# Kernel tuning notes

Hardware: AMD Instinct MI355X
Metric: run time of the kernel (lower is better)

Reference implementation:

```python
import jax, jax.numpy as jnp
import numpy as np

D = 128
H = 4
DK = D // H


def _spmm(row, col, val, x, n):
    # sparse.mm(adj, x) with adj in COO form: out[row] += val * x[col]
    return jax.ops.segment_sum(val[:, None] * x[col], row, num_segments=n)


def _arrg(h, a1_w, a1_b, a2_w, a2_b):
    return jax.nn.leaky_relu(h @ a1_w + a1_b, negative_slope=0.01) @ a2_w + a2_b


def _cross_attn(x, q_x, q_w, k_w, v_w):
    n, d = x.shape
    m = q_x.shape[0]
    q = (q_x @ q_w).reshape(m, H, DK).transpose(1, 0, 2)   # [H, Q, dk]
    k = (x @ k_w).reshape(n, H, DK).transpose(1, 0, 2)     # [H, N, dk]
    v = (q_x @ v_w).reshape(m, H, DK).transpose(1, 0, 2)   # [H, Q, dk]
    s = jnp.einsum('hnd,hqd->hnq', k, q) / jnp.sqrt(jnp.float32(DK))
    w = jax.nn.softmax(s, axis=-1)                          # softmax over queries
    out = jnp.einsum('hnq,hqd->hnd', w, v).transpose(1, 0, 2).reshape(n, d)
    return out + x


def setup_inputs() -> dict:
    key = jax.random.key(0)
    ks = iter(jax.random.split(key, 64))
    nrm = lambda shape, s=0.05: jax.random.normal(next(ks), shape, jnp.float32) * s
    inp = {}
    inp['trans_w'] = nrm((1, D)); inp['trans_b'] = nrm((D,))
    inp['g_w'] = nrm((D, D));     inp['g_b'] = nrm((D,))
    inp['qg_w'] = nrm((D, D));    inp['qg_b'] = nrm((D,))
    inp['q_w'] = nrm((D, D)); inp['k_w'] = nrm((D, D)); inp['v_w'] = nrm((D, D))
    inp['a1_w'] = nrm((D, 2 * D)); inp['a1_b'] = nrm((2 * D,))
    inp['a2_w'] = nrm((2 * D, D)); inp['a2_b'] = nrm((D,))
    inp['x0'] = jax.random.normal(next(ks), (25000,), jnp.float32)
    inp['q0'] = jax.random.normal(next(ks), (100,), jnp.float32)
    for i in (1, 2, 3):
        inp[f'xin{i}'] = jax.random.normal(next(ks), (25000,), jnp.float32)
        inp[f'qin{i}'] = jax.random.normal(next(ks), (100,), jnp.float32)
    n_sizes = {1: 50000, 2: 75000, 3: 100000}
    q_sizes = {1: 200, 2: 300, 3: 400}
    for i in (1, 2, 3):
        e = 16 * n_sizes[i]
        inp[f'aval{i}'] = jax.random.uniform(next(ks), (e,), jnp.float32)
        inp[f'arow{i}'] = jax.random.randint(next(ks), (e,), 0, n_sizes[i], jnp.int64)
        inp[f'acol{i}'] = jax.random.randint(next(ks), (e,), 0, n_sizes[i], jnp.int64)
        qe = 16 * q_sizes[i]
        inp[f'qval{i}'] = jax.random.uniform(next(ks), (qe,), jnp.float32)
        inp[f'qrow{i}'] = jax.random.randint(next(ks), (qe,), 0, q_sizes[i], jnp.int64)
        inp[f'qcol{i}'] = jax.random.randint(next(ks), (qe,), 0, q_sizes[i], jnp.int64)
    return inp


def reference(trans_w, trans_b, g_w, g_b, qg_w, qg_b, q_w, k_w, v_w,
              a1_w, a1_b, a2_w, a2_b,
              x0, q0, xin1, xin2, xin3, qin1, qin2, qin3,
              aval1, aval2, aval3, qval1, qval2, qval3,
              arow1, acol1, arow2, acol2, arow3, acol3,
              qrow1, qcol1, qrow2, qcol2, qrow3, qcol3):
    trans = lambda v: v[:, None] @ trans_w + trans_b
    x = trans(x0)
    qx = trans(q0)
    steps = [
        (xin1, qin1, arow1, acol1, aval1, qrow1, qcol1, qval1, 50000, 200),
        (xin2, qin2, arow2, acol2, aval2, qrow2, qcol2, qval2, 75000, 300),
        (xin3, qin3, arow3, acol3, aval3, qrow3, qcol3, qval3, 100000, 400),
    ]
    for xin, qin, ar, ac, av, qr, qc, qv, n, m in steps:
        x = jnp.concatenate([x, trans(xin)], axis=0)
        qx = jnp.concatenate([qx, trans(qin)], axis=0)
        x = _spmm(ar, ac, av, x @ g_w + g_b, n)
        qx = _spmm(qr, qc, qv, qx @ qg_w + qg_b, m)
        x = _arrg(x, a1_w, a1_b, a2_w, a2_b)
        qx = _arrg(qx, a1_w, a1_b, a2_w, a2_b)
        x = _cross_attn(x, qx, q_w, k_w, v_w)
    return (x, qx)
```

## Files before the change

### kernel.cpp

```cpp
#include <hip/hip_runtime.h>

typedef unsigned short u16;
typedef __attribute__((ext_vector_type(8))) short bf16x8;
typedef __attribute__((ext_vector_type(4))) float f32x4;
typedef __attribute__((ext_vector_type(2))) unsigned u32x2;

__device__ __forceinline__ float b2f(u16 v) {
    return __uint_as_float(((unsigned)v) << 16);
}
__device__ __forceinline__ u16 f2b(float x) {
    unsigned u = __float_as_uint(x);
    unsigned r = u + 0x7FFFu + ((u >> 16) & 1u);
    return (u16)(r >> 16);
}
__device__ __forceinline__ float4 load_bf4(const u16* p) {
    ushort4 q = *(const ushort4*)p;
    float4 f;
    f.x = b2f(q.x); f.y = b2f(q.y); f.z = b2f(q.z); f.w = b2f(q.w);
    return f;
}
__device__ __forceinline__ float4 in4(const void* p, long off, bool bf) {
    if (bf) return load_bf4((const u16*)p + off);
    return *(const float4*)((const float*)p + off);
}
__device__ __forceinline__ float in1(const void* p, long off, bool bf) {
    if (bf) return b2f(((const u16*)p)[off]);
    return ((const float*)p)[off];
}
__device__ __forceinline__ int inIdx(const void* p, long i, bool i64) {
    return ((const int*)p)[i64 ? 2 * i : i];
}

__global__ void sniff_kernel(const u16* __restrict__ x0bits, const int* __restrict__ arow,
                             int* __restrict__ flags) {
    if (threadIdx.x != 0 || blockIdx.x != 0) return;
    int plaus = 0;
    for (int i = 0; i < 256; ++i) {
        u16 v = x0bits[i];
        int e = (v >> 7) & 0xFF;
        if (v == 0 || (e >= 100 && e <= 135)) plaus++;
    }
    flags[0] = (plaus >= 200) ? 1 : 0;
    int nz = 0;
    for (int i = 1; i < 128; i += 2) nz += (arow[i] != 0);
    flags[1] = (nz == 0) ? 1 : 0;
}

__global__ void trans2_kernel(const void* __restrict__ vx, float* __restrict__ outx, int rowsx,
                              const void* __restrict__ vq, float* __restrict__ outq, int rowsq,
                              const void* __restrict__ tw, const void* __restrict__ tb,
                              const int* __restrict__ flags) {
    const bool bf = flags[0] != 0;
    int t = blockIdx.x * blockDim.x + threadIdx.x;
    int c4 = (t & 31) * 4;
    int r = t >> 5;
    const void* v; float* out;
    if (r < rowsx) { v = vx; out = outx; }
    else { r -= rowsx; if (r >= rowsq) return; v = vq; out = outq; }
    float vv = in1(v, r, bf);
    float4 w4 = in4(tw, c4, bf);
    float4 b4 = in4(tb, c4, bf);
    float4 o;
    o.x = vv * w4.x + b4.x; o.y = vv * w4.y + b4.y;
    o.z = vv * w4.z + b4.z; o.w = vv * w4.w + b4.w;
    *(float4*)(out + (size_t)r * 128 + c4) = o;
}

__global__ void wprep_kernel(const void* __restrict__ src, u16* __restrict__ dst,
                             int K, int N, const int* __restrict__ flags) {
    const bool bf = flags[0] != 0;
    int idx = blockIdx.x * blockDim.x + threadIdx.x;
    if (idx >= K * N) return;
    int j = idx & 7, lane = (idx >> 3) & 63, t = idx >> 9;
    int KC = K >> 5;
    int kc = t % KC, ct = t / KC;
    int k = kc * 32 + (lane >> 4) * 8 + j;
    int nn = ct * 16 + (lane & 15);
    dst[idx] = f2b(in1(src, (long)k * N + nn, bf));
}

template<int KTOT, int NOUT, bool LEAKY, typename AT, typename CT>
__launch_bounds__(256)
__global__ void gemm_mfma_kernel(const AT* __restrict__ A, const u16* __restrict__ Wf,
                                 const void* __restrict__ bias, CT* __restrict__ C,
                                 int n, const int* __restrict__ flags) {
    constexpr int KC = KTOT / 32;
    constexpr int NT = NOUT / 16;
    __shared__ u16 wlds[KTOT * NOUT];
    {
        const int4* srcw = (const int4*)Wf;
        int4* dstw = (int4*)wlds;
        constexpr int NV = KTOT * NOUT * 2 / 16;
#pragma unroll
        for (int i = 0; i < NV / 256; ++i)
            dstw[i * 256 + threadIdx.x] = srcw[i * 256 + threadIdx.x];
    }
    __syncthreads();
    const bool bf = flags[0] != 0;
    const int lane = threadIdx.x & 63;
    const int wave = threadIdx.x >> 6;
    const int quad = lane >> 4, col = lane & 15;
    const int rbase = (blockIdx.x * 4 + wave) * 16;
    if (rbase >= n) return;
    int node = rbase + col; if (node >= n) node = n - 1;
    f32x4 acc[NT];
#pragma unroll
    for (int ct = 0; ct < NT; ++ct) acc[ct] = (f32x4){0.f, 0.f, 0.f, 0.f};
#pragma unroll
    for (int kc = 0; kc < KC; ++kc) {
        bf16x8 af;
        if constexpr (sizeof(AT) == 2) {
            af = *(const bf16x8*)((const u16*)A + (size_t)node * KTOT + kc * 32 + quad * 8);
        } else {
            const float* ap = (const float*)A + (size_t)node * KTOT + kc * 32 + quad * 8;
            float4 a0 = *(const float4*)ap;
            float4 a1 = *(const float4*)(ap + 4);
            af[0] = (short)f2b(a0.x); af[1] = (short)f2b(a0.y);
            af[2] = (short)f2b(a0.z); af[3] = (short)f2b(a0.w);
            af[4] = (short)f2b(a1.x); af[5] = (short)f2b(a1.y);
            af[6] = (short)f2b(a1.z); af[7] = (short)f2b(a1.w);
        }
#pragma unroll
        for (int ct = 0; ct < NT; ++ct) {
            bf16x8 wf = *(const bf16x8*)(wlds + (((ct * KC + kc) * 64 + lane) * 8));
            acc[ct] = __builtin_amdgcn_mfma_f32_16x16x32_bf16(af, wf, acc[ct], 0, 0, 0);
        }
    }
#pragma unroll
    for (int ct = 0; ct < NT; ++ct) {
        int colg = ct * 16 + col;
        float b = bias ? in1(bias, colg, bf) : 0.f;
#pragma unroll
        for (int r = 0; r < 4; ++r) {
            int row = rbase + quad * 4 + r;
            if (row >= n) continue;
            float v = acc[ct][r] + b;
            if (LEAKY) v = v > 0.f ? v : 0.01f * v;
            if constexpr (sizeof(CT) == 2) C[(size_t)row * NOUT + colg] = (CT)f2b(v);
            else                           C[(size_t)row * NOUT + colg] = (CT)v;
        }
    }
}

__launch_bounds__(256)
__global__ void gemm_qv_kernel(const float* __restrict__ A, const u16* __restrict__ Wfq,
                               const u16* __restrict__ Wfv, u16* __restrict__ Qf,
                               u16* __restrict__ Vf, int m, int mt32) {
    __shared__ u16 wldsq[128 * 128];
    __shared__ u16 wldsv[128 * 128];
    {
        const int4* sq = (const int4*)Wfq;
        const int4* sv = (const int4*)Wfv;
        int4* dq = (int4*)wldsq;
        int4* dv = (int4*)wldsv;
#pragma unroll
        for (int i = 0; i < 8; ++i) {
            dq[i * 256 + threadIdx.x] = sq[i * 256 + threadIdx.x];
            dv[i * 256 + threadIdx.x] = sv[i * 256 + threadIdx.x];
        }
    }
    __syncthreads();
    const int mpad = mt32 * 32;
    const int mt16 = mt32 * 2;
    const int lane = threadIdx.x & 63;
    const int wave = threadIdx.x >> 6;
    const int quad = lane >> 4, col = lane & 15;
    const int rbase = (blockIdx.x * 4 + wave) * 16;
    if (rbase >= mpad) return;
    int node = rbase + col; if (node >= m) node = m - 1;
    f32x4 accq[8], accv[8];
#pragma unroll
    for (int ct = 0; ct < 8; ++ct) {
        accq[ct] = (f32x4){0.f, 0.f, 0.f, 0.f};
        accv[ct] = (f32x4){0.f, 0.f, 0.f, 0.f};
    }
#pragma unroll
    for (int kc = 0; kc < 4; ++kc) {
        const float* ap = A + (size_t)node * 128 + kc * 32 + quad * 8;
        float4 a0 = *(const float4*)ap;
        float4 a1 = *(const float4*)(ap + 4);
        bf16x8 af;
        af[0] = (short)f2b(a0.x); af[1] = (short)f2b(a0.y);
        af[2] = (short)f2b(a0.z); af[3] = (short)f2b(a0.w);
        af[4] = (short)f2b(a1.x); af[5] = (short)f2b(a1.y);
        af[6] = (short)f2b(a1.z); af[7] = (short)f2b(a1.w);
#pragma unroll
        for (int ct = 0; ct < 8; ++ct) {
            bf16x8 wq = *(const bf16x8*)(wldsq + (((ct * 4 + kc) * 64 + lane) * 8));
            bf16x8 wv = *(const bf16x8*)(wldsv + (((ct * 4 + kc) * 64 + lane) * 8));
            accq[ct] = __builtin_amdgcn_mfma_f32_16x16x32_bf16(af, wq, accq[ct], 0, 0, 0);
            accv[ct] = __builtin_amdgcn_mfma_f32_16x16x32_bf16(af, wv, accv[ct], 0, 0, 0);
        }
    }
    const float qscale = 0.17677669529663687f * 1.44269504088896340736f;
#pragma unroll
    for (int ct = 0; ct < 8; ++ct) {
        int colg = ct * 16 + col;
        int h = colg >> 5, dim = colg & 31;
#pragma unroll
        for (int r = 0; r < 4; ++r) {
            int row = rbase + quad * 4 + r;
            if (row >= mpad) continue;
            bool pad = row >= m;
            float vq = pad ? 0.f : accq[ct][r] * qscale;
            float vv = pad ? 0.f : accv[ct][r];
            {
                size_t idx = ((((size_t)h * mt16 + (row >> 4)) * 64)
                              + ((dim >> 3) << 4) + (row & 15)) * 8 + (dim & 7);
                Qf[idx] = f2b(vq);
            }
            {
                size_t idx = (((((size_t)h * mt32 + (row >> 5)) * 2 + (dim >> 4)) * 64)
                              + (((row >> 3) & 3) << 4) + (dim & 15)) * 8 + (row & 7);
                Vf[idx] = f2b(vv);
            }
        }
    }
}

#define RSH 8
#define NBC_MAX 512
#define EPB 4096

__global__ void zero_int_kernel(int* __restrict__ p, int n) {
    int i = blockIdx.x * blockDim.x + threadIdx.x;
    if (i < n) p[i] = 0;
}

__global__ void bhist_kernel(const void* __restrict__ rows, int e, int* __restrict__ bcnt,
                             int nbc, const int* __restrict__ flags) {
    __shared__ int hist[NBC_MAX];
    const bool i64 = flags[1] != 0;
    for (int i = threadIdx.x; i < nbc; i += 256) hist[i] = 0;
    __syncthreads();
    int base = blockIdx.x * 8192;
    int end = base + 8192; if (end > e) end = e;
    for (int i = base + threadIdx.x; i < end; i += 256)
        atomicAdd(&hist[inIdx(rows, i, i64) >> RSH], 1);
    __syncthreads();
    for (int i = threadIdx.x; i < nbc; i += 256) {
        int c = hist[i];
        if (c) atomicAdd(&bcnt[i], c);
    }
}

__global__ void scanF_kernel(const int* __restrict__ bcnt, int nbc,
                             int* __restrict__ optr, int* __restrict__ ocur) {
    __shared__ int sc[NBC_MAX];
    const int tid = threadIdx.x;
    int v0 = (tid < nbc) ? bcnt[tid] : 0;
    int v1 = (tid + 256 < nbc) ? bcnt[tid + 256] : 0;
    sc[tid] = v0; sc[tid + 256] = v1;
    __syncthreads();
    for (int off = 1; off < NBC_MAX; off <<= 1) {
        int a = (tid >= off) ? sc[tid - off] : 0;
        int b = sc[tid + 256 - off];
        __syncthreads();
        sc[tid] += a;
        sc[tid + 256] += b;
        __syncthreads();
    }
    if (tid < nbc)       { int x = sc[tid] - v0;       optr[tid] = x;       ocur[tid] = x; }
    if (tid + 256 < nbc) { int x = sc[tid + 256] - v1; optr[tid + 256] = x; ocur[tid + 256] = x; }
}

__launch_bounds__(256)
__global__ void qbuild_kernel(const void* __restrict__ rows, const void* __restrict__ colsin,
                              const void* __restrict__ valsin, int e, int nrows,
                              int2* __restrict__ pack1, int* __restrict__ rowptr,
                              int* __restrict__ rowend, const int* __restrict__ flags) {
    __shared__ int hist[512], cur[512], sc[512];
    const bool bf = flags[0] != 0;
    const bool i64 = flags[1] != 0;
    const int tid = threadIdx.x;
    for (int i = tid; i < 512; i += 256) hist[i] = 0;
    __syncthreads();
    for (int i = tid; i < e; i += 256)
        atomicAdd(&hist[inIdx(rows, i, i64)], 1);
    __syncthreads();
    int v0 = hist[tid], v1 = hist[tid + 256];
    sc[tid] = v0; sc[tid + 256] = v1;
    __syncthreads();
    for (int off = 1; off < 512; off <<= 1) {
        int a = (tid >= off) ? sc[tid - off] : 0;
        int b = sc[tid + 256 - off];
        __syncthreads();
        sc[tid] += a;
        sc[tid + 256] += b;
        __syncthreads();
    }
    {
        int x = sc[tid] - v0;
        cur[tid] = x;
        if (tid < nrows) { rowptr[tid] = x; rowend[tid] = x + v0; }
        int x1 = sc[tid + 256] - v1;
        cur[tid + 256] = x1;
        if (tid + 256 < nrows) { rowptr[tid + 256] = x1; rowend[tid + 256] = x1 + v1; }
    }
    __syncthreads();
    for (int i = tid; i < e; i += 256) {
        int r = inIdx(rows, i, i64);
        int p = atomicAdd(&cur[r], 1);
        pack1[p] = (int2){inIdx(colsin, i, i64), __float_as_int(in1(valsin, i, bf))};
    }
}

__launch_bounds__(256)
__global__ void psort_kernel(const void* __restrict__ rows, const void* __restrict__ colsin,
                             const void* __restrict__ valsin, int e,
                             int* __restrict__ gcur, int2* __restrict__ pack0,
                             int nbc, const int* __restrict__ flags) {
    __shared__ int hist[NBC_MAX];
    __shared__ int scan[NBC_MAX];
    __shared__ int base[NBC_MAX];
    __shared__ int cur[NBC_MAX];
    __shared__ int2 stage[EPB];
    __shared__ u16 binof[EPB];
    const bool bf = flags[0] != 0;
    const bool i64 = flags[1] != 0;
    const int tid = threadIdx.x;
    const long s0 = (long)blockIdx.x * EPB;
    int cnt_e = e - (int)s0; if (cnt_e > EPB) cnt_e = EPB;

    for (int i = tid; i < NBC_MAX; i += 256) hist[i] = 0;
    __syncthreads();
    for (int j = tid; j < cnt_e; j += 256)
        atomicAdd(&hist[inIdx(rows, s0 + j, i64) >> RSH], 1);
    __syncthreads();
    for (int i = tid; i < NBC_MAX; i += 256) scan[i] = hist[i];
    __syncthreads();
    for (int off = 1; off < NBC_MAX; off <<= 1) {
        int a = (tid >= off) ? scan[tid - off] : 0;
        int c = scan[tid + 256 - off];
        __syncthreads();
        scan[tid] += a;
        scan[tid + 256] += c;
        __syncthreads();
    }
    for (int i = tid; i < nbc; i += 256) {
        int h = hist[i];
        cur[i] = scan[i] - h;
        base[i] = h ? atomicAdd(&gcur[i], h) : 0;
    }
    __syncthreads();
    for (int j = tid; j < cnt_e; j += 256) {
        int r = inIdx(rows, s0 + j, i64);
        int bin = r >> RSH;
        int p = atomicAdd(&cur[bin], 1);
        int2 pk;
        pk.x = ((r & ((1 << RSH) - 1)) << 20) | inIdx(colsin, s0 + j, i64);
        pk.y = __float_as_int(in1(valsin, s0 + j, bf));
        stage[p] = pk;
        binof[p] = (u16)bin;
    }
    __syncthreads();
    for (int j = tid; j < cnt_e; j += 256) {
        int bin = binof[j];
        int st = scan[bin] - hist[bin];
        pack0[base[bin] + (j - st)] = stage[j];
    }
}

__launch_bounds__(256)
__global__ void breorder256_kernel(const int2* __restrict__ pack0, const int* __restrict__ bptr,
                                   const int* __restrict__ bend, int2* __restrict__ pack1,
                                   int* __restrict__ rowptr, int* __restrict__ rowend, int n) {
    __shared__ int hist[256], scan[256], cur[256];
    const int b = blockIdx.x;
    const int s = bptr[b], e = bend[b];
    const int tid = threadIdx.x;
    hist[tid] = 0;
    __syncthreads();
    for (int i = s + tid; i < e; i += 256)
        atomicAdd(&hist[(unsigned)pack0[i].x >> 20], 1);
    __syncthreads();
    scan[tid] = hist[tid];
    __syncthreads();
    for (int off = 1; off < 256; off <<= 1) {
        int a = (tid >= off) ? scan[tid - off] : 0;
        __syncthreads();
        scan[tid] += a;
        __syncthreads();
    }
    int st = s + scan[tid] - hist[tid];
    cur[tid] = st;
    int rg = (b << RSH) + tid;
    if (rg < n) { rowptr[rg] = st; rowend[rg] = st + hist[tid]; }
    __syncthreads();
    for (int i = s + tid; i < e; i += 256) {
        int2 pk = pack0[i];
        int rl = (unsigned)pk.x >> 20;
        int p = atomicAdd(&cur[rl], 1);
        pack1[p] = (int2){pk.x & 0xFFFFF, pk.y};
    }
}

__device__ __forceinline__ void bffma8(float v, uint4 h, float* a) {
    a[0] += v * __uint_as_float(h.x << 16);
    a[1] += v * __uint_as_float(h.x & 0xFFFF0000u);
    a[2] += v * __uint_as_float(h.y << 16);
    a[3] += v * __uint_as_float(h.y & 0xFFFF0000u);
    a[4] += v * __uint_as_float(h.z << 16);
    a[5] += v * __uint_as_float(h.z & 0xFFFF0000u);
    a[6] += v * __uint_as_float(h.w << 16);
    a[7] += v * __uint_as_float(h.w & 0xFFFF0000u);
}
__global__ void spmm_kernel(const u16* __restrict__ H, const int* __restrict__ rowptr,
                            const int* __restrict__ rowend, const int2* __restrict__ pack,
                            u16* __restrict__ out, int n) {
    int w = threadIdx.x >> 6;
    int lane = threadIdx.x & 63;
    int r = blockIdx.x * 4 + w;
    if (r >= n) return;
    const int s16 = lane >> 4;
    const int l16 = lane & 15;
    int s = rowptr[r], e = rowend[r];
    float a[8] = {0.f, 0.f, 0.f, 0.f, 0.f, 0.f, 0.f, 0.f};
    int i = s + s16;
    for (; i + 12 < e; i += 16) {
        int2 p0 = pack[i], p1 = pack[i + 4], p2 = pack[i + 8], p3 = pack[i + 12];
        uint4 h0 = *(const uint4*)(H + (size_t)p0.x * 128 + l16 * 8);
        uint4 h1 = *(const uint4*)(H + (size_t)p1.x * 128 + l16 * 8);
        uint4 h2 = *(const uint4*)(H + (size_t)p2.x * 128 + l16 * 8);
        uint4 h3 = *(const uint4*)(H + (size_t)p3.x * 128 + l16 * 8);
        bffma8(__int_as_float(p0.y), h0, a);
        bffma8(__int_as_float(p1.y), h1, a);
        bffma8(__int_as_float(p2.y), h2, a);
        bffma8(__int_as_float(p3.y), h3, a);
    }
    for (; i < e; i += 4) {
        int2 p0 = pack[i];
        uint4 h0 = *(const uint4*)(H + (size_t)p0.x * 128 + l16 * 8);
        bffma8(__int_as_float(p0.y), h0, a);
    }
#pragma unroll
    for (int k = 0; k < 8; ++k) {
        a[k] += __shfl_xor(a[k], 16, 64);
        a[k] += __shfl_xor(a[k], 32, 64);
    }
    if (s16 == 0) {
        uint4 o;
        o.x = (unsigned)f2b(a[0]) | ((unsigned)f2b(a[1]) << 16);
        o.y = (unsigned)f2b(a[2]) | ((unsigned)f2b(a[3]) << 16);
        o.z = (unsigned)f2b(a[4]) | ((unsigned)f2b(a[5]) << 16);
        o.w = (unsigned)f2b(a[6]) | ((unsigned)f2b(a[7]) << 16);
        *(uint4*)(out + (size_t)r * 128 + l16 * 8) = o;
    }
}

__launch_bounds__(256)
__global__ void attn_mfma_kernel(const u16* __restrict__ Kb, const u16* __restrict__ Qf,
                                 const u16* __restrict__ Vf, float* __restrict__ X,
                                 int n, int m, int mt32, int pad) {
    __shared__ __align__(128) u16 Pbuf_all[4 * 1024];
    const int h = blockIdx.y;
    const int wave = threadIdx.x >> 6;
    const int lane = threadIdx.x & 63;
    const int nb = (blockIdx.x * 4 + wave) * 32;
    if (nb >= n) return;
    const int quad = lane >> 4, col = lane & 15;
    int node0 = nb + col;      if (node0 >= n) node0 = n - 1;
    int node1 = nb + 16 + col; if (node1 >= n) node1 = n - 1;
    bf16x8 kf0 = *(const bf16x8*)(Kb + (size_t)node0 * 128 + h * 32 + quad * 8);
    bf16x8 kf1 = *(const bf16x8*)(Kb + (size_t)node1 * 128 + h * 32 + quad * 8);
    f32x4 O00 = {0.f, 0.f, 0.f, 0.f}, O01 = {0.f, 0.f, 0.f, 0.f};
    f32x4 O10 = {0.f, 0.f, 0.f, 0.f}, O11 = {0.f, 0.f, 0.f, 0.f};
    const f32x4 zero = {0.f, 0.f, 0.f, 0.f};
    float Lp0[4] = {0.f, 0.f, 0.f, 0.f};
    float Lp1[4] = {0.f, 0.f, 0.f, 0.f};
    u16* Pw0 = Pbuf_all + wave * 1024;
    u16* Pw1 = Pw0 + 512;
    uint2* pw0[2]; uint2* pw1[2];
    pw0[0] = (uint2*)(Pw0 + col * 16 + quad * 4);
    pw0[1] = (uint2*)(Pw0 + 256 + col * 16 + quad * 4);
    pw1[0] = (uint2*)(Pw1 + col * 16 + quad * 4);
    pw1[1] = (uint2*)(Pw1 + 256 + col * 16 + quad * 4);
    const unsigned paddr0 = (unsigned)(uintptr_t)Pw0 + (unsigned)(quad * 256 + col * 8);
    const unsigned paddr1 = (unsigned)(uintptr_t)Pw1 + (unsigned)(quad * 256 + col * 8);
    const u16* Qbase = Qf + (size_t)h * (mt32 * 2) * 512;
    const u16* Vbase = Vf + (size_t)h * mt32 * 1024;
    for (int qc = 0; qc < mt32; ++qc) {
#pragma unroll
        for (int half = 0; half < 2; ++half) {
            bf16x8 qfr = *(const bf16x8*)(Qbase + (size_t)(qc * 2 + half) * 512 + lane * 8);
            f32x4 S0 = __builtin_amdgcn_mfma_f32_16x16x32_bf16(kf0, qfr, zero, 0, 0, 0);
            f32x4 S1 = __builtin_amdgcn_mfma_f32_16x16x32_bf16(kf1, qfr, zero, 0, 0, 0);
            float a0 = __builtin_amdgcn_exp2f(fminf(S0[0], 115.f));
            float a1 = __builtin_amdgcn_exp2f(fminf(S0[1], 115.f));
            float a2 = __builtin_amdgcn_exp2f(fminf(S0[2], 115.f));
            float a3 = __builtin_amdgcn_exp2f(fminf(S0[3], 115.f));
            float b0 = __builtin_amdgcn_exp2f(fminf(S1[0], 115.f));
            float b1 = __builtin_amdgcn_exp2f(fminf(S1[1], 115.f));
            float b2 = __builtin_amdgcn_exp2f(fminf(S1[2], 115.f));
            float b3 = __builtin_amdgcn_exp2f(fminf(S1[3], 115.f));
            Lp0[0] += a0; Lp0[1] += a1; Lp0[2] += a2; Lp0[3] += a3;
            Lp1[0] += b0; Lp1[1] += b1; Lp1[2] += b2; Lp1[3] += b3;
            unsigned ra, rb, rc, rd;
            asm volatile("v_cvt_pk_bf16_f32 %0, %1, %2" : "=v"(ra) : "v"(a0), "v"(a1));
            asm volatile("v_cvt_pk_bf16_f32 %0, %1, %2" : "=v"(rb) : "v"(a2), "v"(a3));
            asm volatile("v_cvt_pk_bf16_f32 %0, %1, %2" : "=v"(rc) : "v"(b0), "v"(b1));
            asm volatile("v_cvt_pk_bf16_f32 %0, %1, %2" : "=v"(rd) : "v"(b2), "v"(b3));
            uint2 pka; pka.x = ra; pka.y = rb;
            uint2 pkb; pkb.x = rc; pkb.y = rd;
            *pw0[half] = pka;
            *pw1[half] = pkb;
        }
        asm volatile("s_waitcnt lgkmcnt(0)" ::: "memory");
        u32x2 t0a, t0b, t1a, t1b;
        asm volatile("ds_read_b64_tr_b16 %0, %1" : "=&v"(t0a) : "v"(paddr0) : "memory");
        asm volatile("ds_read_b64_tr_b16 %0, %1 offset:128" : "=&v"(t0b) : "v"(paddr0) : "memory");
        asm volatile("ds_read_b64_tr_b16 %0, %1" : "=&v"(t1a) : "v"(paddr1) : "memory");
        asm volatile("ds_read_b64_tr_b16 %0, %1 offset:128" : "=&v"(t1b) : "v"(paddr1) : "memory");
        asm volatile("s_waitcnt lgkmcnt(0)" ::: "memory");
        __builtin_amdgcn_sched_barrier(0);
        bf16x8 pf0, pf1;
        ((u32x2*)&pf0)[0] = t0a; ((u32x2*)&pf0)[1] = t0b;
        ((u32x2*)&pf1)[0] = t1a; ((u32x2*)&pf1)[1] = t1b;
        bf16x8 v0 = *(const bf16x8*)(Vbase + (size_t)(qc * 2 + 0) * 512 + lane * 8);
        bf16x8 v1 = *(const bf16x8*)(Vbase + (size_t)(qc * 2 + 1) * 512 + lane * 8);
        __builtin_amdgcn_s_setprio(1);
        O00 = __builtin_amdgcn_mfma_f32_16x16x32_bf16(pf0, v0, O00, 0, 0, 0);
        O01 = __builtin_amdgcn_mfma_f32_16x16x32_bf16(pf0, v1, O01, 0, 0, 0);
        O10 = __builtin_amdgcn_mfma_f32_16x16x32_bf16(pf1, v0, O10, 0, 0, 0);
        O11 = __builtin_amdgcn_mfma_f32_16x16x32_bf16(pf1, v1, O11, 0, 0, 0);
        __builtin_amdgcn_s_setprio(0);
    }
#pragma unroll
    for (int mask = 1; mask < 16; mask <<= 1) {
#pragma unroll
        for (int r = 0; r < 4; ++r) {
            Lp0[r] += __shfl_xor(Lp0[r], mask, 64);
            Lp1[r] += __shfl_xor(Lp1[r], mask, 64);
        }
    }
#pragma unroll
    for (int r = 0; r < 4; ++r) {
        int nd = nb + quad * 4 + r;
        if (nd < n) {
            float inv = 1.f / fmaxf(Lp0[r] - (float)pad, 1e-35f);
            float* xp = X + (size_t)nd * 128 + h * 32;
            xp[col]      += O00[r] * inv;
            xp[16 + col] += O01[r] * inv;
        }
        int nd1 = nb + 16 + quad * 4 + r;
        if (nd1 < n) {
            float inv = 1.f / fmaxf(Lp1[r] - (float)pad, 1e-35f);
            float* xp = X + (size_t)nd1 * 128 + h * 32;
            xp[col]      += O10[r] * inv;
            xp[16 + col] += O11[r] * inv;
        }
    }
}

__global__ void out_writer_kernel(const float* __restrict__ in, void* __restrict__ out,
                                  long elem_off, int n4, const int* __restrict__ flags) {
    const bool bf = flags[0] != 0;
    int i = blockIdx.x * blockDim.x + threadIdx.x;
    if (i >= n4) return;
    float4 v = ((const float4*)in)[i];
    if (bf) {
        ushort4 q; q.x = f2b(v.x); q.y = f2b(v.y); q.z = f2b(v.z); q.w = f2b(v.w);
        ((ushort4*)((u16*)out + elem_off))[i] = q;
    } else {
        ((float4*)((float*)out + elem_off))[i] = v;
    }
}

extern "C" void kernel_launch(void* const* d_in, const int* in_sizes, int n_in,
                              void* d_out, int out_size, void* d_ws, size_t ws_size,
                              hipStream_t stream) {
    (void)n_in; (void)out_size; (void)ws_size;
    const void* trans_w = d_in[0];
    const void* trans_b = d_in[1];
    const void* g_w  = d_in[2];
    const void* g_b  = d_in[3];
    const void* qg_w = d_in[4];
    const void* qg_b = d_in[5];
    const void* q_w  = d_in[6];
    const void* k_w  = d_in[7];
    const void* v_w  = d_in[8];
    const void* a1_w = d_in[9];
    const void* a1_b = d_in[10];
    const void* a2_w = d_in[11];
    const void* a2_b = d_in[12];
    const void* x0   = d_in[13];
    const void* q0   = d_in[14];

    int ixin[3], iqin[3], iaval[3], iarow[3], iacol[3], iqval[3], iqrow[3], iqcol[3];
    if (in_sizes[16] == 100) {
        for (int s = 0; s < 3; ++s) {
            ixin[s] = 15 + 2 * s; iqin[s] = 16 + 2 * s;
            int b = 21 + 6 * s;
            iaval[s] = b; iarow[s] = b + 1; iacol[s] = b + 2;
            iqval[s] = b + 3; iqrow[s] = b + 4; iqcol[s] = b + 5;
        }
    } else {
        int xs[3] = {15,16,17}, qs_[3] = {18,19,20};
        int av[3] = {21,22,23}, qv[3] = {24,25,26};
        int ar[3] = {27,29,31}, ac[3] = {28,30,32};
        int qr[3] = {33,35,37}, qc[3] = {34,36,38};
        for (int s = 0; s < 3; ++s) {
            ixin[s]=xs[s]; iqin[s]=qs_[s]; iaval[s]=av[s]; iqval[s]=qv[s];
            iarow[s]=ar[s]; iacol[s]=ac[s]; iqrow[s]=qr[s]; iqcol[s]=qc[s];
        }
    }

    char* p = (char*)d_ws;
    auto alloc = [&](size_t bytes) -> char* {
        char* r = p;
        p += (bytes + 255) & ~(size_t)255;
        return r;
    };
    int*   flags = (int*)alloc(256);
    const int NMAX = 100000;
    float* X   = (float*)alloc((size_t)NMAX * 128 * 4);
    u16*   T1b = (u16*)  alloc((size_t)NMAX * 128 * 2);
    u16*   Xs  = (u16*)  alloc((size_t)NMAX * 128 * 2);
    u16*   T2  = (u16*)  alloc((size_t)NMAX * 256 * 2);
    float* QX  = (float*)alloc((size_t)400 * 128 * 4);
    u16*   QT1b= (u16*)  alloc((size_t)400 * 128 * 2);
    u16*   QXs = (u16*)  alloc((size_t)400 * 128 * 2);
    u16*   QT2 = (u16*)  alloc((size_t)400 * 256 * 2);
    u16*   Qfrag = (u16*)alloc((size_t)4 * 13 * 1024 * 2);
    u16*   Vfrag = (u16*)alloc((size_t)4 * 13 * 1024 * 2);
    u16* Wg  = (u16*)alloc((size_t)128 * 128 * 2);
    u16* Wqg = (u16*)alloc((size_t)128 * 128 * 2);
    u16* Wa1 = (u16*)alloc((size_t)128 * 256 * 2);
    u16* Wa2 = (u16*)alloc((size_t)256 * 128 * 2);
    u16* Wk  = (u16*)alloc((size_t)128 * 128 * 2);
    u16* Wq  = (u16*)alloc((size_t)128 * 128 * 2);
    u16* Wv  = (u16*)alloc((size_t)128 * 128 * 2);
    int2*  csr_pack = (int2*)alloc((size_t)1600000 * 8);
    int*   bcnt   = (int*)alloc((size_t)NBC_MAX * 4);
    int*   bktptr = (int*)alloc((size_t)NBC_MAX * 4);
    int*   bktcur = (int*)alloc((size_t)NBC_MAX * 4);
    int*   rowptr = (int*)alloc((size_t)NMAX * 4);
    int*   rowend = (int*)alloc((size_t)NMAX * 4);
    int2*  pack0  = (int2*)T2;

    sniff_kernel<<<1, 64, 0, stream>>>((const u16*)x0, (const int*)d_in[iarow[0]], flags);

    auto wprep = [&](const void* src, u16* dst, int K, int N) {
        wprep_kernel<<<(K * N + 255) / 256, 256, 0, stream>>>(src, dst, K, N, flags);
    };
    wprep(g_w,  Wg,  128, 128);
    wprep(qg_w, Wqg, 128, 128);
    wprep(a1_w, Wa1, 128, 256);
    wprep(a2_w, Wa2, 256, 128);
    wprep(k_w,  Wk,  128, 128);
    wprep(q_w,  Wq,  128, 128);
    wprep(v_w,  Wv,  128, 128);

    auto launch_trans2 = [&](const void* vx, float* outx, int rowsx,
                             const void* vq, float* outq, int rowsq) {
        int tot = (rowsx + rowsq) * 32;
        trans2_kernel<<<(tot + 255) / 256, 256, 0, stream>>>(vx, outx, rowsx,
                                                             vq, outq, rowsq,
                                                             trans_w, trans_b, flags);
    };
    auto build_spmm = [&](const void* rows, const void* colsidx, const void* vals, int e,
                          int nrows, const u16* H, u16* OUT) {
        if (nrows <= 512) {
            qbuild_kernel<<<1, 256, 0, stream>>>(rows, colsidx, vals, e, nrows,
                                                 csr_pack, rowptr, rowend, flags);
        } else {
            int nbc = (nrows + 255) >> RSH;
            zero_int_kernel<<<(nbc + 255) / 256, 256, 0, stream>>>(bcnt, nbc);
            bhist_kernel<<<(e + 8191) / 8192, 256, 0, stream>>>(rows, e, bcnt, nbc, flags);
            scanF_kernel<<<1, 256, 0, stream>>>(bcnt, nbc, bktptr, bktcur);
            psort_kernel<<<(e + EPB - 1) / EPB, 256, 0, stream>>>(rows, colsidx, vals, e,
                                                                  bktcur, pack0, nbc, flags);
            breorder256_kernel<<<nbc, 256, 0, stream>>>(pack0, bktptr, bktcur, csr_pack,
                                                        rowptr, rowend, nrows);
        }
        spmm_kernel<<<(nrows + 3) / 4, 256, 0, stream>>>(H, rowptr, rowend, csr_pack,
                                                         OUT, nrows);
    };

    int nprev = in_sizes[13];
    int mprev = in_sizes[14];
    launch_trans2(x0, X, nprev, q0, QX, mprev);

    const int ns[3] = {50000, 75000, 100000};
    const int ms[3] = {200, 300, 400};
    for (int s = 0; s < 3; ++s) {
        const int n = ns[s], m = ms[s];
        const int e  = in_sizes[iaval[s]];
        const int qe = in_sizes[iqval[s]];
        launch_trans2(d_in[ixin[s]], X + (size_t)nprev * 128, n - nprev,
                      d_in[iqin[s]], QX + (size_t)mprev * 128, m - mprev);
        const int gb  = (n + 63) / 64;
        const int gqb = (m + 63) / 64;
        gemm_mfma_kernel<128, 128, false, float, u16><<<gb, 256, 0, stream>>>(X, Wg, g_b, T1b, n, flags);
        build_spmm(d_in[iarow[s]], d_in[iacol[s]], d_in[iaval[s]], e, n, T1b, Xs);
        gemm_mfma_kernel<128, 128, false, float, u16><<<gqb, 256, 0, stream>>>(QX, Wqg, qg_b, QT1b, m, flags);
        build_spmm(d_in[iqrow[s]], d_in[iqcol[s]], d_in[iqval[s]], qe, m, QT1b, QXs);
        gemm_mfma_kernel<128, 256, true, u16, u16><<<gb, 256, 0, stream>>>(Xs, Wa1, a1_b, T2, n, flags);
        gemm_mfma_kernel<256, 128, false, u16, float><<<gb, 256, 0, stream>>>(T2, Wa2, a2_b, X, n, flags);
        gemm_mfma_kernel<128, 256, true, u16, u16><<<gqb, 256, 0, stream>>>(QXs, Wa1, a1_b, QT2, m, flags);
        gemm_mfma_kernel<256, 128, false, u16, float><<<gqb, 256, 0, stream>>>(QT2, Wa2, a2_b, QX, m, flags);
        const int mt32 = (m + 31) / 32;
        const int pad = mt32 * 32 - m;
        gemm_mfma_kernel<128, 128, false, float, u16><<<gb, 256, 0, stream>>>(X, Wk, nullptr, T1b, n, flags);
        gemm_qv_kernel<<<(mt32 * 32 + 63) / 64, 256, 0, stream>>>(QX, Wq, Wv, Qfrag, Vfrag, m, mt32);
        attn_mfma_kernel<<<dim3((n + 127) / 128, 4), 256, 0, stream>>>(T1b, Qfrag, Vfrag, X, n, m, mt32, pad);
        nprev = n;
        mprev = m;
    }

    const int n4x = 100000 * 128 / 4;
    const int n4q = 400 * 128 / 4;
    out_writer_kernel<<<(n4x + 255) / 256, 256, 0, stream>>>(X, d_out, 0, n4x, flags);
    out_writer_kernel<<<(n4q + 255) / 256, 256, 0, stream>>>(QX, d_out, (long)100000 * 128, n4q, flags);
}
```

Baseline: 1.211 ms.

## Use fixed-stride row buckets to drop histogram/scan passes and merge launches

```diff
diff --git a/kernel.cpp b/kernel.cpp
--- a/kernel.cpp
+++ b/kernel.cpp
@@ -66,17 +66,35 @@
     *(float4*)(out + (size_t)r * 128 + c4) = o;
 }
 
-__global__ void wprep_kernel(const void* __restrict__ src, u16* __restrict__ dst,
-                             int K, int N, const int* __restrict__ flags) {
+__global__ void wprep_all_kernel(const void* __restrict__ g_w, const void* __restrict__ qg_w,
+                                 const void* __restrict__ a1_w, const void* __restrict__ a2_w,
+                                 const void* __restrict__ k_w, const void* __restrict__ q_w,
+                                 const void* __restrict__ v_w,
+                                 u16* __restrict__ Wg, u16* __restrict__ Wqg,
+                                 u16* __restrict__ Wa1, u16* __restrict__ Wa2,
+                                 u16* __restrict__ Wk, u16* __restrict__ Wq,
+                                 u16* __restrict__ Wv, const int* __restrict__ flags) {
     const bool bf = flags[0] != 0;
     int idx = blockIdx.x * blockDim.x + threadIdx.x;
-    if (idx >= K * N) return;
-    int j = idx & 7, lane = (idx >> 3) & 63, t = idx >> 9;
+    const void* src; u16* dst; int K, N, loc;
+    if (idx < 32768) {
+        if (idx < 16384) { src = g_w; dst = Wg; loc = idx; }
+        else { src = qg_w; dst = Wqg; loc = idx - 16384; }
+        K = 128; N = 128;
+    } else if (idx < 65536) { src = a1_w; dst = Wa1; loc = idx - 32768; K = 128; N = 256; }
+    else if (idx < 98304)  { src = a2_w; dst = Wa2; loc = idx - 65536; K = 256; N = 128; }
+    else if (idx < 147456) {
+        if (idx < 114688) { src = k_w; dst = Wk; loc = idx - 98304; }
+        else if (idx < 131072) { src = q_w; dst = Wq; loc = idx - 114688; }
+        else { src = v_w; dst = Wv; loc = idx - 131072; }
+        K = 128; N = 128;
+    } else return;
+    int j = loc & 7, lane = (loc >> 3) & 63, t = loc >> 9;
     int KC = K >> 5;
     int kc = t % KC, ct = t / KC;
     int k = kc * 32 + (lane >> 4) * 8 + j;
     int nn = ct * 16 + (lane & 15);
-    dst[idx] = f2b(in1(src, (long)k * N + nn, bf));
+    dst[loc] = f2b(in1(src, (long)k * N + nn, bf));
 }
 
 template<int KTOT, int NOUT, bool LEAKY, typename AT, typename CT>
@@ -221,47 +239,11 @@
 #define RSH 8
 #define NBC_MAX 512
 #define EPB 4096
-
-__global__ void zero_int_kernel(int* __restrict__ p, int n) {
+#define BSTRIDE 6144
+
+__global__ void ginit_kernel(int* __restrict__ p, int nbc) {
     int i = blockIdx.x * blockDim.x + threadIdx.x;
-    if (i < n) p[i] = 0;
-}
-
-__global__ void bhist_kernel(const void* __restrict__ rows, int e, int* __restrict__ bcnt,
-                             int nbc, const int* __restrict__ flags) {
-    __shared__ int hist[NBC_MAX];
-    const bool i64 = flags[1] != 0;
-    for (int i = threadIdx.x; i < nbc; i += 256) hist[i] = 0;
-    __syncthreads();
-    int base = blockIdx.x * 8192;
-    int end = base + 8192; if (end > e) end = e;
-    for (int i = base + threadIdx.x; i < end; i += 256)
-        atomicAdd(&hist[inIdx(rows, i, i64) >> RSH], 1);
-    __syncthreads();
-    for (int i = threadIdx.x; i < nbc; i += 256) {
-        int c = hist[i];
-        if (c) atomicAdd(&bcnt[i], c);
-    }
-}
-
-__global__ void scanF_kernel(const int* __restrict__ bcnt, int nbc,
-                             int* __restrict__ optr, int* __restrict__ ocur) {
-    __shared__ int sc[NBC_MAX];
-    const int tid = threadIdx.x;
-    int v0 = (tid < nbc) ? bcnt[tid] : 0;
-    int v1 = (tid + 256 < nbc) ? bcnt[tid + 256] : 0;
-    sc[tid] = v0; sc[tid + 256] = v1;
-    __syncthreads();
-    for (int off = 1; off < NBC_MAX; off <<= 1) {
-        int a = (tid >= off) ? sc[tid - off] : 0;
-        int b = sc[tid + 256 - off];
-        __syncthreads();
-        sc[tid] += a;
-        sc[tid + 256] += b;
-        __syncthreads();
-    }
-    if (tid < nbc)       { int x = sc[tid] - v0;       optr[tid] = x;       ocur[tid] = x; }
-    if (tid + 256 < nbc) { int x = sc[tid + 256] - v1; optr[tid + 256] = x; ocur[tid + 256] = x; }
+    if (i < nbc) p[i] = i * BSTRIDE;
 }
 
 __launch_bounds__(256)
@@ -362,12 +344,12 @@
 }
 
 __launch_bounds__(256)
-__global__ void breorder256_kernel(const int2* __restrict__ pack0, const int* __restrict__ bptr,
-                                   const int* __restrict__ bend, int2* __restrict__ pack1,
+__global__ void breorder256_kernel(const int2* __restrict__ pack0, const int* __restrict__ bend,
+                                   int2* __restrict__ pack1,
                                    int* __restrict__ rowptr, int* __restrict__ rowend, int n) {
     __shared__ int hist[256], scan[256], cur[256];
     const int b = blockIdx.x;
-    const int s = bptr[b], e = bend[b];
+    const int s = b * BSTRIDE, e = bend[b];
     const int tid = threadIdx.x;
     hist[tid] = 0;
     __syncthreads();
@@ -552,17 +534,19 @@
     }
 }
 
-__global__ void out_writer_kernel(const float* __restrict__ in, void* __restrict__ out,
-                                  long elem_off, int n4, const int* __restrict__ flags) {
+__global__ void out_writer_kernel(const float* __restrict__ X, const float* __restrict__ QX,
+                                  void* __restrict__ out, const int* __restrict__ flags) {
     const bool bf = flags[0] != 0;
+    const int n4x = 100000 * 128 / 4;
+    const int n4t = n4x + 400 * 128 / 4;
     int i = blockIdx.x * blockDim.x + threadIdx.x;
-    if (i >= n4) return;
-    float4 v = ((const float4*)in)[i];
+    if (i >= n4t) return;
+    float4 v = (i < n4x) ? ((const float4*)X)[i] : ((const float4*)QX)[i - n4x];
     if (bf) {
         ushort4 q; q.x = f2b(v.x); q.y = f2b(v.y); q.z = f2b(v.z); q.w = f2b(v.w);
-        ((ushort4*)((u16*)out + elem_off))[i] = q;
+        ((ushort4*)out)[i] = q;
     } else {
-        ((float4*)((float*)out + elem_off))[i] = v;
+        ((float4*)out)[i] = v;
     }
 }
 
@@ -613,6 +597,7 @@
     };
     int*   flags = (int*)alloc(256);
     const int NMAX = 100000;
+    const int NBINS = (NMAX + 255) >> RSH;
     float* X   = (float*)alloc((size_t)NMAX * 128 * 4);
     u16*   T1b = (u16*)  alloc((size_t)NMAX * 128 * 2);
     u16*   Xs  = (u16*)  alloc((size_t)NMAX * 128 * 2);
@@ -630,9 +615,7 @@
     u16* Wk  = (u16*)alloc((size_t)128 * 128 * 2);
     u16* Wq  = (u16*)alloc((size_t)128 * 128 * 2);
     u16* Wv  = (u16*)alloc((size_t)128 * 128 * 2);
-    int2*  csr_pack = (int2*)alloc((size_t)1600000 * 8);
-    int*   bcnt   = (int*)alloc((size_t)NBC_MAX * 4);
-    int*   bktptr = (int*)alloc((size_t)NBC_MAX * 4);
+    int2*  csr_pack = (int2*)alloc((size_t)(NBINS + 1) * BSTRIDE * 8);
     int*   bktcur = (int*)alloc((size_t)NBC_MAX * 4);
     int*   rowptr = (int*)alloc((size_t)NMAX * 4);
     int*   rowend = (int*)alloc((size_t)NMAX * 4);
@@ -640,16 +623,9 @@
 
     sniff_kernel<<<1, 64, 0, stream>>>((const u16*)x0, (const int*)d_in[iarow[0]], flags);
 
-    auto wprep = [&](const void* src, u16* dst, int K, int N) {
-        wprep_kernel<<<(K * N + 255) / 256, 256, 0, stream>>>(src, dst, K, N, flags);
-    };
-    wprep(g_w,  Wg,  128, 128);
-    wprep(qg_w, Wqg, 128, 128);
-    wprep(a1_w, Wa1, 128, 256);
-    wprep(a2_w, Wa2, 256, 128);
-    wprep(k_w,  Wk,  128, 128);
-    wprep(q_w,  Wq,  128, 128);
-    wprep(v_w,  Wv,  128, 128);
+    wprep_all_kernel<<<(147456 + 255) / 256, 256, 0, stream>>>(
+        g_w, qg_w, a1_w, a2_w, k_w, q_w, v_w,
+        Wg, Wqg, Wa1, Wa2, Wk, Wq, Wv, flags);
 
     auto launch_trans2 = [&](const void* vx, float* outx, int rowsx,
                              const void* vq, float* outq, int rowsq) {
@@ -665,12 +641,10 @@
                                                  csr_pack, rowptr, rowend, flags);
         } else {
             int nbc = (nrows + 255) >> RSH;
-            zero_int_kernel<<<(nbc + 255) / 256, 256, 0, stream>>>(bcnt, nbc);
-            bhist_kernel<<<(e + 8191) / 8192, 256, 0, stream>>>(rows, e, bcnt, nbc, flags);
-            scanF_kernel<<<1, 256, 0, stream>>>(bcnt, nbc, bktptr, bktcur);
+            ginit_kernel<<<(nbc + 255) / 256, 256, 0, stream>>>(bktcur, nbc);
             psort_kernel<<<(e + EPB - 1) / EPB, 256, 0, stream>>>(rows, colsidx, vals, e,
                                                                   bktcur, pack0, nbc, flags);
-            breorder256_kernel<<<nbc, 256, 0, stream>>>(pack0, bktptr, bktcur, csr_pack,
+            breorder256_kernel<<<nbc, 256, 0, stream>>>(pack0, bktcur, csr_pack,
                                                         rowptr, rowend, nrows);
         }
         spmm_kernel<<<(nrows + 3) / 4, 256, 0, stream>>>(H, rowptr, rowend, csr_pack,
@@ -708,8 +682,6 @@
         mprev = m;
     }
 
-    const int n4x = 100000 * 128 / 4;
-    const int n4q = 400 * 128 / 4;
-    out_writer_kernel<<<(n4x + 255) / 256, 256, 0, stream>>>(X, d_out, 0, n4x, flags);
-    out_writer_kernel<<<(n4q + 255) / 256, 256, 0, stream>>>(QX, d_out, (long)100000 * 128, n4q, flags);
-}
+    const int n4t = (100000 + 400) * 128 / 4;
+    out_writer_kernel<<<(n4t + 255) / 256, 256, 0, stream>>>(X, QX, d_out, flags);
+}
```

Result: faster. 1.144 ms (-5.5%).
